# Optimization experiments

Hardware: AMD Instinct MI355X
Metric: run time of the kernel (lower is better)

Reference implementation:

```python
import jax, jax.numpy as jnp
import numpy as np

B, L, E, H = 2, 4096, 1024, 16
D = E // H          # head_dim = 64
CHUNK = 256         # matches the torch module's chunk_size


def setup_inputs() -> dict:
    key = jax.random.key(0)
    k1, k2, k3 = jax.random.split(key, 3)
    x = jax.random.normal(k1, (B, L, E), dtype=jnp.float32)
    # torch Linear weight layout: (out_features, in_features); y = x @ W.T
    W_qkv = jax.random.normal(k2, (3 * E, E), dtype=jnp.float32) * 0.02
    W_out = jax.random.normal(k3, (E, E), dtype=jnp.float32) * 0.02
    return {"x": x, "W_qkv": W_qkv, "W_out": W_out}


def _linear_attention(x, W_qkv, W_out):
    Bz, Lz, Ez = x.shape
    scale = D ** (-0.5)
    qkv = x @ W_qkv.T                                # [B, L, 3E]
    qkv = qkv.reshape(Bz, Lz, 3, H, D).transpose(2, 0, 3, 1, 4)  # [3, B, H, L, D]
    q, k, v = qkv[0], qkv[1], qkv[2]
    # feature map: elu(x) + 1, query also scaled by head_dim^-0.5
    q = (jax.nn.elu(q) + 1.0) * scale
    k = jax.nn.elu(k) + 1.0

    nc = Lz // CHUNK  # seq_len chosen divisible by CHUNK
    def to_chunks(t):  # [B,H,L,D] -> [nc, B, H, CHUNK, D]
        return t.reshape(Bz, H, nc, CHUNK, D).transpose(2, 0, 1, 3, 4)
    qc, kc, vc = to_chunks(q), to_chunks(k), to_chunks(v)

    causal = jnp.tril(jnp.ones((CHUNK, CHUNK), dtype=x.dtype))

    def step(carry, inp):
        S, Z = carry                     # S: [B,H,D,D], Z: [B,H,D]
        qi, ki, vi = inp                 # each [B,H,CHUNK,D]
        # intra-chunk causal contribution (same math as cumsum of k v^T outer products)
        attn = jnp.einsum('bhld,bhmd->bhlm', qi, ki) * causal
        num = jnp.einsum('bhlm,bhme->bhle', attn, vi) + jnp.einsum('bhld,bhde->bhle', qi, S)
        den = attn.sum(-1) + jnp.einsum('bhld,bhd->bhl', qi, Z)
        S = S + jnp.einsum('bhmd,bhme->bhde', ki, vi)
        Z = Z + ki.sum(axis=2)
        return (S, Z), (num, den)

    S0 = jnp.zeros((Bz, H, D, D), dtype=x.dtype)
    Z0 = jnp.zeros((Bz, H, D), dtype=x.dtype)
    _, (num, den) = jax.lax.scan(step, (S0, Z0), (qc, kc, vc))
    # [nc,B,H,CHUNK,D] -> [B,H,L,D]
    num = num.transpose(1, 2, 0, 3, 4).reshape(Bz, H, Lz, D)
    den = den.transpose(1, 2, 0, 3).reshape(Bz, H, Lz)
    den = jnp.maximum(den, 1e-6)
    out = num / den[..., None]
    out = out.transpose(0, 2, 1, 3).reshape(Bz, Lz, Ez)
    return out @ W_out.T


def reference(x, W_qkv, W_out):
    return _linear_attention(x, W_qkv, W_out)
```

## Files before the change

### kernel.cpp

```cpp
#include <hip/hip_runtime.h>
#include <hip/hip_bf16.h>
#include <math.h>

#define B_ 2
#define L_ 4096
#define E_ 1024
#define H_ 16
#define D_ 64
#define CK_ 64
#define NC_ 64

typedef __bf16 bf16x8 __attribute__((ext_vector_type(8)));
typedef __bf16 bf16x4 __attribute__((ext_vector_type(4)));
typedef float  f32x4  __attribute__((ext_vector_type(4)));

__device__ __forceinline__ float fmap1(float x) { return x > 0.f ? x + 1.f : expf(x); }
__device__ __forceinline__ float b2f(__bf16 v) {
    __hip_bfloat16 h = *reinterpret_cast<__hip_bfloat16*>(&v); return __bfloat162float(h);
}
__device__ __forceinline__ __bf16 f2b(float f) {
    __hip_bfloat16 h = __float2bfloat16(f); return *reinterpret_cast<__bf16*>(&h);
}
__device__ __forceinline__ unsigned short f2u(float f) {
    __hip_bfloat16 h = __float2bfloat16(f); return *reinterpret_cast<unsigned short*>(&h);
}

union U8 { bf16x8 v; __bf16 e[8]; bf16x4 half2[2]; };

__device__ __forceinline__ void async16(const __bf16* g, __bf16* lds) {
    __builtin_amdgcn_global_load_lds(
        (const __attribute__((address_space(1))) void*)g,
        (__attribute__((address_space(3))) void*)lds, 16, 0, 0);
}

__global__ __launch_bounds__(256) void cast_f32_bf16(const float* __restrict__ in,
                                                     __hip_bfloat16* __restrict__ out, int n) {
    int i = (blockIdx.x * 256 + threadIdx.x) << 2;
    if (i < n) {
        float4 v = *(const float4*)(in + i);
        ushort4 o = {f2u(v.x), f2u(v.y), f2u(v.z), f2u(v.w)};
        *(ushort4*)(out + i) = o;
    }
}

#define WVMC(n) do { asm volatile("s_waitcnt vmcnt(" #n ")" ::: "memory"); \
    __builtin_amdgcn_sched_barrier(0); } while (0)

template<int EPI>
__global__ __launch_bounds__(256) void gemm_mfma3(const __bf16* __restrict__ A,
                                                  const __bf16* __restrict__ Bw,
                                                  void* __restrict__ Cv,
                                                  __hip_bfloat16* __restrict__ KT,
                                                  __hip_bfloat16* __restrict__ VT,
                                                  int M, int N, int K) {
    __shared__ alignas(16) __bf16 As[3][128 * 32];
    __shared__ alignas(16) __bf16 Bs[3][128 * 32];
    const int tid = threadIdx.x;
    const int wave = tid >> 6, lane = tid & 63;
    const int wm = wave >> 1, wn = wave & 1;
    const int lq = lane >> 4, lr = lane & 15;
    const int m0 = blockIdx.y * 128, n0 = blockIdx.x * 128;
    const int NS = K >> 5;

    f32x4 acc[4][4];
#pragma unroll
    for (int i = 0; i < 4; ++i)
#pragma unroll
        for (int j = 0; j < 4; ++j) acc[i][j] = (f32x4){0.f, 0.f, 0.f, 0.f};

    const int stg_r = lane >> 2, stg_c = (lane & 3) << 3;
    const __bf16* Ag0 = A + (size_t)(m0 + (wave << 4) + stg_r) * K + stg_c;
    const __bf16* Ag1 = A + (size_t)(m0 + 64 + (wave << 4) + stg_r) * K + stg_c;
    const __bf16* Bg0 = Bw + (size_t)(n0 + (wave << 4) + stg_r) * K + stg_c;
    const __bf16* Bg1 = Bw + (size_t)(n0 + 64 + (wave << 4) + stg_r) * K + stg_c;
    const int dl0 = (wave << 9), dl1 = ((wave + 4) << 9);

#define STG3(bi, t) do { const int ko_ = (t) << 5; \
    async16(Ag0 + ko_, &As[bi][dl0]); \
    async16(Ag1 + ko_, &As[bi][dl1]); \
    async16(Bg0 + ko_, &Bs[bi][dl0]); \
    async16(Bg1 + ko_, &Bs[bi][dl1]); } while (0)

    STG3(0, 0);
    STG3(1, 1);
    WVMC(4);
    __builtin_amdgcn_s_barrier();

    int bi = 0, bn = 2;
    for (int t = 0; t < NS; ++t) {
        if (t + 2 < NS) STG3(bn, t + 2);
        bf16x8 af[4], bfr[4];
#pragma unroll
        for (int tt = 0; tt < 4; ++tt) {
            af[tt]  = *(const bf16x8*)&As[bi][((wm << 6) + (tt << 4) + lr) * 32 + (lq << 3)];
            bfr[tt] = *(const bf16x8*)&Bs[bi][((wn << 6) + (tt << 4) + lr) * 32 + (lq << 3)];
        }
#pragma unroll
        for (int mt = 0; mt < 4; ++mt)
#pragma unroll
            for (int nt = 0; nt < 4; ++nt)
                acc[mt][nt] = __builtin_amdgcn_mfma_f32_16x16x32_bf16(
                    af[mt], bfr[nt], acc[mt][nt], 0, 0, 0);
        if (t < NS - 2)       { WVMC(4); }
        else if (t == NS - 2) { WVMC(0); }
        __builtin_amdgcn_s_barrier();
        bi = (bi == 2) ? 0 : bi + 1;
        bn = (bn == 2) ? 0 : bn + 1;
    }

#pragma unroll
    for (int mt = 0; mt < 4; ++mt) {
#pragma unroll
        for (int nt = 0; nt < 4; ++nt) {
            int m = m0 + (wm << 6) + (mt << 4) + (lq << 2);
            int n = n0 + (wn << 6) + (nt << 4) + lr;
            if (EPI == 1) {
                int w = n >> 10, hh = (n >> 6) & 15, dd = n & 63;
                float vv[4];
#pragma unroll
                for (int r = 0; r < 4; ++r) {
                    float v = acc[mt][nt][r];
                    if (w == 0)      v = fmap1(v) * 0.125f;
                    else if (w == 1) v = fmap1(v);
                    vv[r] = v;
                    ((__hip_bfloat16*)Cv)[(size_t)(m + r) * N + n] = __float2bfloat16(v);
                }
                if (w >= 1) {
                    int b = m >> 12, l = m & 4095;
                    __hip_bfloat16* T = (w == 1) ? KT : VT;
                    ushort4 u = {f2u(vv[0]), f2u(vv[1]), f2u(vv[2]), f2u(vv[3])};
                    *(ushort4*)&T[((size_t)((b * 16 + hh) * 64 + dd) << 12) + l] = u;
                }
            } else {
#pragma unroll
                for (int r = 0; r < 4; ++r)
                    ((float*)Cv)[(size_t)(m + r) * N + n] = acc[mt][nt][r];
            }
        }
    }
#undef STG3
}

__global__ __launch_bounds__(256) void chunk_state_mfma(const __hip_bfloat16* __restrict__ KTh,
                                                        const __hip_bfloat16* __restrict__ VTh,
                                                        __hip_bfloat16* __restrict__ Sb,
                                                        __hip_bfloat16* __restrict__ Zb) {
    const int tid = threadIdx.x, wave = tid >> 6, lane = tid & 63;
    const int quad = lane >> 4, lr = lane & 15;
    const int bh = blockIdx.y;
    const int c = blockIdx.x * 4 + wave;
    const __bf16* KT = (const __bf16*)KTh;
    const __bf16* VT = (const __bf16*)VTh;

    bf16x8 vt[4][2], kt[4][2];
#pragma unroll
    for (int t = 0; t < 4; ++t)
#pragma unroll
        for (int kk = 0; kk < 2; ++kk) {
            size_t rowoff = ((size_t)(bh * 64 + t * 16 + lr) << 12) + c * CK_ + kk * 32 + quad * 8;
            vt[t][kk] = *(const bf16x8*)&VT[rowoff];
            kt[t][kk] = *(const bf16x8*)&KT[rowoff];
        }

    U8 of;
#pragma unroll
    for (int j = 0; j < 8; ++j) of.e[j] = f2b(1.0f);

    __hip_bfloat16* Sp = Sb + ((size_t)(c * 32 + bh) << 12);
#pragma unroll
    for (int es = 0; es < 4; ++es) {
#pragma unroll
        for (int dt = 0; dt < 4; ++dt) {
            f32x4 acc = (f32x4){0.f, 0.f, 0.f, 0.f};
            acc = __builtin_amdgcn_mfma_f32_16x16x32_bf16(vt[es][0], kt[dt][0], acc, 0, 0, 0);
            acc = __builtin_amdgcn_mfma_f32_16x16x32_bf16(vt[es][1], kt[dt][1], acc, 0, 0, 0);
#pragma unroll
            for (int r = 0; r < 4; ++r)
                Sp[(es * 16 + quad * 4 + r) * 64 + dt * 16 + lr] =
                    __float2bfloat16(acc[r]);
        }
    }
#pragma unroll
    for (int dt = 0; dt < 4; ++dt) {
        f32x4 z = (f32x4){0.f, 0.f, 0.f, 0.f};
        z = __builtin_amdgcn_mfma_f32_16x16x32_bf16(kt[dt][0], of.v, z, 0, 0, 0);
        z = __builtin_amdgcn_mfma_f32_16x16x32_bf16(kt[dt][1], of.v, z, 0, 0, 0);
        if (lr == 0) {
#pragma unroll
            for (int r = 0; r < 4; ++r)
                Zb[((c * 32 + bh) << 6) + dt * 16 + quad * 4 + r] = __float2bfloat16(z[r]);
        }
    }
}

__global__ __launch_bounds__(256) void prefix64(__hip_bfloat16* __restrict__ Sb,
                                                __hip_bfloat16* __restrict__ Zb) {
    const int bh = blockIdx.y;
    const int idx = blockIdx.x * 256 + threadIdx.x;
    float run = 0.f;
    for (int c = 0; c < NC_; ++c) {
        size_t off = ((size_t)(c * 32 + bh) << 12) + idx;
        float cur = __bfloat162float(Sb[off]);
        Sb[off] = __float2bfloat16(run);
        run += cur;
    }
    if (blockIdx.x == 0 && threadIdx.x < 64) {
        float zr = 0.f;
        for (int c = 0; c < NC_; ++c) {
            int zoff = ((c * 32 + bh) << 6) + threadIdx.x;
            float cz = __bfloat162float(Zb[zoff]);
            Zb[zoff] = __float2bfloat16(zr);
            zr += cz;
        }
    }
}

__global__ __launch_bounds__(256) void attn_out_mfma(const __hip_bfloat16* __restrict__ qvh,
                                                     const __hip_bfloat16* __restrict__ Sbh,
                                                     const __hip_bfloat16* __restrict__ Zbh,
                                                     const __hip_bfloat16* __restrict__ VTh,
                                                     __hip_bfloat16* __restrict__ attn) {
    __shared__ __bf16 Pbuf[4 * 64 * 68];
    const int tid = threadIdx.x, wave = tid >> 6, lane = tid & 63;
    const int quad = lane >> 4, lr = lane & 15;
    const int bh = blockIdx.y, b = bh >> 4, h = bh & 15;
    const int c = blockIdx.x * 4 + wave;
    const size_t t0 = (size_t)b * L_ + c * CK_;
    const __bf16* qb = (const __bf16*)qvh;
    const __bf16* Sb = (const __bf16*)Sbh;
    const __bf16* Zb = (const __bf16*)Zbh;
    const __bf16* VT = (const __bf16*)VTh;
    __bf16* P = Pbuf + wave * (64 * 68);

    bf16x8 qf[4][2];
#pragma unroll
    for (int ls = 0; ls < 4; ++ls)
#pragma unroll
        for (int kk = 0; kk < 2; ++kk)
            qf[ls][kk] = *(const bf16x8*)&qb[(t0 + ls * 16 + lr) * 3072 + h * 64 + kk * 32 + quad * 8];

    f32x4 num[4][4], den[4];
#pragma unroll
    for (int i = 0; i < 4; ++i) {
        den[i] = (f32x4){0.f, 0.f, 0.f, 0.f};
#pragma unroll
        for (int j = 0; j < 4; ++j) num[i][j] = (f32x4){0.f, 0.f, 0.f, 0.f};
    }

    bf16x8 zf[2];
#pragma unroll
    for (int kk = 0; kk < 2; ++kk)
        zf[kk] = *(const bf16x8*)&Zb[((size_t)(c * 32 + bh) << 6) + kk * 32 + quad * 8];
#pragma unroll
    for (int ls = 0; ls < 4; ++ls)
#pragma unroll
        for (int kk = 0; kk < 2; ++kk)
            den[ls] = __builtin_amdgcn_mfma_f32_16x16x32_bf16(qf[ls][kk], zf[kk], den[ls], 0, 0, 0);

#pragma unroll
    for (int es = 0; es < 4; ++es) {
        bf16x8 sf[2];
#pragma unroll
        for (int kk = 0; kk < 2; ++kk)
            sf[kk] = *(const bf16x8*)&Sb[((size_t)(c * 32 + bh) << 12)
                                         + (es * 16 + lr) * 64 + kk * 32 + quad * 8];
#pragma unroll
        for (int ls = 0; ls < 4; ++ls)
#pragma unroll
            for (int kk = 0; kk < 2; ++kk)
                num[ls][es] = __builtin_amdgcn_mfma_f32_16x16x32_bf16(
                    qf[ls][kk], sf[kk], num[ls][es], 0, 0, 0);
    }

    bf16x8 kf[4][2];
#pragma unroll
    for (int ms = 0; ms < 4; ++ms)
#pragma unroll
        for (int kk = 0; kk < 2; ++kk)
            kf[ms][kk] = *(const bf16x8*)&qb[(t0 + ms * 16 + lr) * 3072 + 1024 + h * 64 + kk * 32 + quad * 8];

#pragma unroll
    for (int ls = 0; ls < 4; ++ls) {
#pragma unroll
        for (int ms = 0; ms < 4; ++ms) {
            int off = (ls * 16 + lr) * 68 + ms * 16 + quad * 4;
            if (ms <= ls) {
                f32x4 pt = (f32x4){0.f, 0.f, 0.f, 0.f};
                pt = __builtin_amdgcn_mfma_f32_16x16x32_bf16(kf[ms][0], qf[ls][0], pt, 0, 0, 0);
                pt = __builtin_amdgcn_mfma_f32_16x16x32_bf16(kf[ms][1], qf[ls][1], pt, 0, 0, 0);
                ushort4 u;
                if (ms == ls) {
                    u.x = (quad * 4 + 0 > lr) ? 0 : f2u(pt[0]);
                    u.y = (quad * 4 + 1 > lr) ? 0 : f2u(pt[1]);
                    u.z = (quad * 4 + 2 > lr) ? 0 : f2u(pt[2]);
                    u.w = (quad * 4 + 3 > lr) ? 0 : f2u(pt[3]);
                } else {
                    u = (ushort4){f2u(pt[0]), f2u(pt[1]), f2u(pt[2]), f2u(pt[3])};
                }
                *(ushort4*)&P[off] = u;
            } else {
                *(ushort4*)&P[off] = (ushort4){0, 0, 0, 0};
            }
        }
    }

    U8 of;
#pragma unroll
    for (int j = 0; j < 8; ++j) of.e[j] = f2b(1.0f);

#pragma unroll
    for (int kk = 0; kk < 2; ++kk) {
        U8 pf[4];
#pragma unroll
        for (int ls = 0; ls < 4; ++ls) {
            pf[ls].half2[0] = *(const bf16x4*)&P[(ls * 16 + lr) * 68 + kk * 32 + quad * 8];
            pf[ls].half2[1] = *(const bf16x4*)&P[(ls * 16 + lr) * 68 + kk * 32 + quad * 8 + 4];
        }
        bf16x8 vf[4];
#pragma unroll
        for (int es = 0; es < 4; ++es)
            vf[es] = *(const bf16x8*)&VT[((size_t)((b * 16 + h) * 64 + es * 16 + lr) << 12)
                                         + c * CK_ + kk * 32 + quad * 8];
#pragma unroll
        for (int ls = 0; ls < 4; ++ls) {
            den[ls] = __builtin_amdgcn_mfma_f32_16x16x32_bf16(pf[ls].v, of.v, den[ls], 0, 0, 0);
#pragma unroll
            for (int es = 0; es < 4; ++es)
                num[ls][es] = __builtin_amdgcn_mfma_f32_16x16x32_bf16(
                    pf[ls].v, vf[es], num[ls][es], 0, 0, 0);
        }
    }

#pragma unroll
    for (int ls = 0; ls < 4; ++ls) {
#pragma unroll
        for (int r = 0; r < 4; ++r) {
            float inv = 1.f / fmaxf(den[ls][r], 1e-6f);
            size_t row = (t0 + ls * 16 + quad * 4 + r) * 1024 + h * 64;
#pragma unroll
            for (int es = 0; es < 4; ++es)
                attn[row + es * 16 + lr] = __float2bfloat16(num[ls][es][r] * inv);
        }
    }
}

extern "C" void kernel_launch(void* const* d_in, const int* in_sizes, int n_in,
                              void* d_out, int out_size, void* d_ws, size_t ws_size,
                              hipStream_t stream) {
    (void)ws_size; (void)out_size;
    const float *x = nullptr, *Wqkv = nullptr, *Wout = nullptr;
    for (int i = 0; i < n_in; ++i) {
        if (in_sizes[i] == 8388608)      x    = (const float*)d_in[i];
        else if (in_sizes[i] == 3145728) Wqkv = (const float*)d_in[i];
        else if (in_sizes[i] == 1048576) Wout = (const float*)d_in[i];
    }

    __hip_bfloat16* ws16  = (__hip_bfloat16*)d_ws;
    __hip_bfloat16* xb    = ws16;
    __hip_bfloat16* attn  = ws16;
    __hip_bfloat16* Wqkvb = ws16 + 8388608;
    __hip_bfloat16* Woutb = Wqkvb + 3145728;
    __hip_bfloat16* qv    = Woutb + 1048576;
    __hip_bfloat16* VT    = qv + 25165824;
    __hip_bfloat16* KT    = VT + 8388608;
    __hip_bfloat16* Sb    = KT + 8388608;
    __hip_bfloat16* Zb    = Sb + 8388608;

    cast_f32_bf16<<<8388608 / 1024, 256, 0, stream>>>(x, xb, 8388608);
    cast_f32_bf16<<<3145728 / 1024, 256, 0, stream>>>(Wqkv, Wqkvb, 3145728);
    cast_f32_bf16<<<1048576 / 1024, 256, 0, stream>>>(Wout, Woutb, 1048576);

    gemm_mfma3<1><<<dim3(3072 / 128, 8192 / 128), 256, 0, stream>>>(
        (const __bf16*)xb, (const __bf16*)Wqkvb, qv, KT, VT, B_ * L_, 3 * E_, E_);
    chunk_state_mfma<<<dim3(16, B_ * H_), 256, 0, stream>>>(KT, VT, Sb, Zb);
    prefix64<<<dim3(16, B_ * H_), 256, 0, stream>>>(Sb, Zb);
    attn_out_mfma<<<dim3(16, B_ * H_), 256, 0, stream>>>(qv, Sb, Zb, VT, attn);
    gemm_mfma3<0><<<dim3(1024 / 128, 8192 / 128), 256, 0, stream>>>(
        (const __bf16*)attn, (const __bf16*)Woutb, d_out, nullptr, nullptr, B_ * L_, E_, E_);
}
```

Before: 244.4 us.

## Load GEMM B operand directly to registers, drop V row-major store, batch prefix loads

The GEMM no longer stages the weight (B) tile through LDS. Each wave loads its B fragments straight from global memory into registers, double-buffered across K steps, while A keeps the async LDS triple buffer. The QKV epilogue now skips writing V into the row-major qkv buffer, since only VT is consumed downstream. The prefix-scan kernel loads all 64 chunk values into registers before writing, so loads are no longer serialized, and launch bounds now ask for 4 blocks per CU. In exchange, B reads become uncached, strided global loads with no LDS sharing between the waves that need the same columns, and register pressure rises.

```diff
diff --git a/kernel.cpp b/kernel.cpp
--- a/kernel.cpp
+++ b/kernel.cpp
@@ -15,9 +15,6 @@
 typedef float  f32x4  __attribute__((ext_vector_type(4)));
 
 __device__ __forceinline__ float fmap1(float x) { return x > 0.f ? x + 1.f : expf(x); }
-__device__ __forceinline__ float b2f(__bf16 v) {
-    __hip_bfloat16 h = *reinterpret_cast<__hip_bfloat16*>(&v); return __bfloat162float(h);
-}
 __device__ __forceinline__ __bf16 f2b(float f) {
     __hip_bfloat16 h = __float2bfloat16(f); return *reinterpret_cast<__bf16*>(&h);
 }
@@ -47,14 +44,13 @@
     __builtin_amdgcn_sched_barrier(0); } while (0)
 
 template<int EPI>
-__global__ __launch_bounds__(256) void gemm_mfma3(const __bf16* __restrict__ A,
+__global__ __launch_bounds__(256, 4) void gemm_bd(const __bf16* __restrict__ A,
                                                   const __bf16* __restrict__ Bw,
                                                   void* __restrict__ Cv,
                                                   __hip_bfloat16* __restrict__ KT,
                                                   __hip_bfloat16* __restrict__ VT,
                                                   int M, int N, int K) {
     __shared__ alignas(16) __bf16 As[3][128 * 32];
-    __shared__ alignas(16) __bf16 Bs[3][128 * 32];
     const int tid = threadIdx.x;
     const int wave = tid >> 6, lane = tid & 63;
     const int wm = wave >> 1, wn = wave & 1;
@@ -71,41 +67,49 @@
     const int stg_r = lane >> 2, stg_c = (lane & 3) << 3;
     const __bf16* Ag0 = A + (size_t)(m0 + (wave << 4) + stg_r) * K + stg_c;
     const __bf16* Ag1 = A + (size_t)(m0 + 64 + (wave << 4) + stg_r) * K + stg_c;
-    const __bf16* Bg0 = Bw + (size_t)(n0 + (wave << 4) + stg_r) * K + stg_c;
-    const __bf16* Bg1 = Bw + (size_t)(n0 + 64 + (wave << 4) + stg_r) * K + stg_c;
     const int dl0 = (wave << 9), dl1 = ((wave + 4) << 9);
 
-#define STG3(bi, t) do { const int ko_ = (t) << 5; \
+    const __bf16* Bp = Bw + (size_t)(n0 + (wn << 6) + lr) * K + (lq << 3);
+
+#define STGA(bi, t) do { const int ko_ = (t) << 5; \
     async16(Ag0 + ko_, &As[bi][dl0]); \
-    async16(Ag1 + ko_, &As[bi][dl1]); \
-    async16(Bg0 + ko_, &Bs[bi][dl0]); \
-    async16(Bg1 + ko_, &Bs[bi][dl1]); } while (0)
-
-    STG3(0, 0);
-    STG3(1, 1);
-    WVMC(4);
+    async16(Ag1 + ko_, &As[bi][dl1]); } while (0)
+#define LDB(dst, t) { const int ko_ = (t) << 5; \
+    _Pragma("unroll") for (int tt = 0; tt < 4; ++tt) \
+        dst[tt] = *(const bf16x8*)&Bp[(size_t)(tt << 4) * K + ko_]; }
+#define LDA_MM(breg) { \
+    bf16x8 af[4]; \
+    _Pragma("unroll") for (int tt = 0; tt < 4; ++tt) \
+        af[tt] = *(const bf16x8*)&As[bi][((wm << 6) + (tt << 4) + lr) * 32 + (lq << 3)]; \
+    _Pragma("unroll") for (int mt = 0; mt < 4; ++mt) \
+    _Pragma("unroll") for (int nt = 0; nt < 4; ++nt) \
+        acc[mt][nt] = __builtin_amdgcn_mfma_f32_16x16x32_bf16( \
+            af[mt], breg[nt], acc[mt][nt], 0, 0, 0); }
+#define ENDSTEP(t) do { \
+    if ((t) < NS - 2)       { WVMC(6); } \
+    else if ((t) == NS - 2) { WVMC(4); } \
+    __builtin_amdgcn_s_barrier(); \
+    bi = (bi == 2) ? 0 : bi + 1; \
+    bn = (bn == 2) ? 0 : bn + 1; } while (0)
+
+    bf16x8 bA[4], bB[4];
+
+    LDB(bA, 0);
+    STGA(0, 0);
+    STGA(1, 1);
+    WVMC(2);
     __builtin_amdgcn_s_barrier();
 
     int bi = 0, bn = 2;
-    for (int t = 0; t < NS; ++t) {
-        if (t + 2 < NS) STG3(bn, t + 2);
-        bf16x8 af[4], bfr[4];
-#pragma unroll
-        for (int tt = 0; tt < 4; ++tt) {
-            af[tt]  = *(const bf16x8*)&As[bi][((wm << 6) + (tt << 4) + lr) * 32 + (lq << 3)];
-            bfr[tt] = *(const bf16x8*)&Bs[bi][((wn << 6) + (tt << 4) + lr) * 32 + (lq << 3)];
-        }
-#pragma unroll
-        for (int mt = 0; mt < 4; ++mt)
-#pragma unroll
-            for (int nt = 0; nt < 4; ++nt)
-                acc[mt][nt] = __builtin_amdgcn_mfma_f32_16x16x32_bf16(
-                    af[mt], bfr[nt], acc[mt][nt], 0, 0, 0);
-        if (t < NS - 2)       { WVMC(4); }
-        else if (t == NS - 2) { WVMC(0); }
-        __builtin_amdgcn_s_barrier();
-        bi = (bi == 2) ? 0 : bi + 1;
-        bn = (bn == 2) ? 0 : bn + 1;
+    for (int t = 0; t < NS; t += 2) {
+        if (t + 1 < NS) LDB(bB, t + 1);
+        if (t + 2 < NS) STGA(bn, t + 2);
+        LDA_MM(bA);
+        ENDSTEP(t);
+        if (t + 2 < NS) LDB(bA, t + 2);
+        if (t + 3 < NS) STGA(bn, t + 3);
+        LDA_MM(bB);
+        ENDSTEP(t + 1);
     }
 
 #pragma unroll
@@ -123,7 +127,8 @@
                     if (w == 0)      v = fmap1(v) * 0.125f;
                     else if (w == 1) v = fmap1(v);
                     vv[r] = v;
-                    ((__hip_bfloat16*)Cv)[(size_t)(m + r) * N + n] = __float2bfloat16(v);
+                    if (w <= 1)
+                        ((__hip_bfloat16*)Cv)[(size_t)(m + r) * N + n] = __float2bfloat16(v);
                 }
                 if (w >= 1) {
                     int b = m >> 12, l = m & 4095;
@@ -138,7 +143,10 @@
             }
         }
     }
-#undef STG3
+#undef STGA
+#undef LDB
+#undef LDA_MM
+#undef ENDSTEP
 }
 
 __global__ __launch_bounds__(256) void chunk_state_mfma(const __hip_bfloat16* __restrict__ KTh,
@@ -197,20 +205,26 @@
                                                 __hip_bfloat16* __restrict__ Zb) {
     const int bh = blockIdx.y;
     const int idx = blockIdx.x * 256 + threadIdx.x;
+    float v[NC_];
+#pragma unroll
+    for (int c = 0; c < NC_; ++c)
+        v[c] = __bfloat162float(Sb[((size_t)(c * 32 + bh) << 12) + idx]);
     float run = 0.f;
+#pragma unroll
     for (int c = 0; c < NC_; ++c) {
-        size_t off = ((size_t)(c * 32 + bh) << 12) + idx;
-        float cur = __bfloat162float(Sb[off]);
-        Sb[off] = __float2bfloat16(run);
-        run += cur;
+        Sb[((size_t)(c * 32 + bh) << 12) + idx] = __float2bfloat16(run);
+        run += v[c];
     }
     if (blockIdx.x == 0 && threadIdx.x < 64) {
+        float z[NC_];
+#pragma unroll
+        for (int c = 0; c < NC_; ++c)
+            z[c] = __bfloat162float(Zb[((c * 32 + bh) << 6) + threadIdx.x]);
         float zr = 0.f;
+#pragma unroll
         for (int c = 0; c < NC_; ++c) {
-            int zoff = ((c * 32 + bh) << 6) + threadIdx.x;
-            float cz = __bfloat162float(Zb[zoff]);
-            Zb[zoff] = __float2bfloat16(zr);
-            zr += cz;
+            Zb[((c * 32 + bh) << 6) + threadIdx.x] = __float2bfloat16(zr);
+            zr += z[c];
         }
     }
 }
@@ -370,11 +384,11 @@
     cast_f32_bf16<<<3145728 / 1024, 256, 0, stream>>>(Wqkv, Wqkvb, 3145728);
     cast_f32_bf16<<<1048576 / 1024, 256, 0, stream>>>(Wout, Woutb, 1048576);
 
-    gemm_mfma3<1><<<dim3(3072 / 128, 8192 / 128), 256, 0, stream>>>(
+    gemm_bd<1><<<dim3(3072 / 128, 8192 / 128), 256, 0, stream>>>(
         (const __bf16*)xb, (const __bf16*)Wqkvb, qv, KT, VT, B_ * L_, 3 * E_, E_);
     chunk_state_mfma<<<dim3(16, B_ * H_), 256, 0, stream>>>(KT, VT, Sb, Zb);
     prefix64<<<dim3(16, B_ * H_), 256, 0, stream>>>(Sb, Zb);
     attn_out_mfma<<<dim3(16, B_ * H_), 256, 0, stream>>>(qv, Sb, Zb, VT, attn);
-    gemm_mfma3<0><<<dim3(1024 / 128, 8192 / 128), 256, 0, stream>>>(
+    gemm_bd<0><<<dim3(1024 / 128, 8192 / 128), 256, 0, stream>>>(
         (const __bf16*)attn, (const __bf16*)Woutb, d_out, nullptr, nullptr, B_ * L_, E_, E_);
 }
```

Measured after the change: 289.1 us. +18.3%, slower.

## Swizzle GEMM block order, skip unused V row-major store, batch prefix loads

Applied to the files above, without the earlier changes.

Remaps GEMM workgroup IDs so consecutive blocks are grouped per XCD (an 8-way interleave), which is meant to improve L2 reuse of A/B tiles. The QKV epilogue no longer writes V into the row-major output, since V is only consumed via the transposed VT buffer. The prefix-sum kernel now issues all 64 chunk loads up front into registers before the serial scan, exposing memory-level parallelism instead of a dependent load/store chain. The remap assumes the block count is divisible by 8, and the register arrays raise VGPR pressure.

```diff
diff --git a/kernel.cpp b/kernel.cpp
--- a/kernel.cpp
+++ b/kernel.cpp
@@ -15,9 +15,6 @@
 typedef float  f32x4  __attribute__((ext_vector_type(4)));
 
 __device__ __forceinline__ float fmap1(float x) { return x > 0.f ? x + 1.f : expf(x); }
-__device__ __forceinline__ float b2f(__bf16 v) {
-    __hip_bfloat16 h = *reinterpret_cast<__hip_bfloat16*>(&v); return __bfloat162float(h);
-}
 __device__ __forceinline__ __bf16 f2b(float f) {
     __hip_bfloat16 h = __float2bfloat16(f); return *reinterpret_cast<__bf16*>(&h);
 }
@@ -59,7 +56,14 @@
     const int wave = tid >> 6, lane = tid & 63;
     const int wm = wave >> 1, wn = wave & 1;
     const int lq = lane >> 4, lr = lane & 15;
-    const int m0 = blockIdx.y * 128, n0 = blockIdx.x * 128;
+
+    const int nwg = gridDim.x * gridDim.y;
+    const int bid = blockIdx.y * gridDim.x + blockIdx.x;
+    const int cpx = nwg >> 3;
+    const int wgid = (bid & 7) * cpx + (bid >> 3);
+    const int bx = wgid % gridDim.x, by = wgid / gridDim.x;
+    const int m0 = by * 128, n0 = bx * 128;
+
     const int NS = K >> 5;
 
     f32x4 acc[4][4];
@@ -123,7 +127,8 @@
                     if (w == 0)      v = fmap1(v) * 0.125f;
                     else if (w == 1) v = fmap1(v);
                     vv[r] = v;
-                    ((__hip_bfloat16*)Cv)[(size_t)(m + r) * N + n] = __float2bfloat16(v);
+                    if (w <= 1)
+                        ((__hip_bfloat16*)Cv)[(size_t)(m + r) * N + n] = __float2bfloat16(v);
                 }
                 if (w >= 1) {
                     int b = m >> 12, l = m & 4095;
@@ -197,20 +202,26 @@
                                                 __hip_bfloat16* __restrict__ Zb) {
     const int bh = blockIdx.y;
     const int idx = blockIdx.x * 256 + threadIdx.x;
+    float v[NC_];
+#pragma unroll
+    for (int c = 0; c < NC_; ++c)
+        v[c] = __bfloat162float(Sb[((size_t)(c * 32 + bh) << 12) + idx]);
     float run = 0.f;
+#pragma unroll
     for (int c = 0; c < NC_; ++c) {
-        size_t off = ((size_t)(c * 32 + bh) << 12) + idx;
-        float cur = __bfloat162float(Sb[off]);
-        Sb[off] = __float2bfloat16(run);
-        run += cur;
+        Sb[((size_t)(c * 32 + bh) << 12) + idx] = __float2bfloat16(run);
+        run += v[c];
     }
     if (blockIdx.x == 0 && threadIdx.x < 64) {
+        float z[NC_];
+#pragma unroll
+        for (int c = 0; c < NC_; ++c)
+            z[c] = __bfloat162float(Zb[((c * 32 + bh) << 6) + threadIdx.x]);
         float zr = 0.f;
+#pragma unroll
         for (int c = 0; c < NC_; ++c) {
-            int zoff = ((c * 32 + bh) << 6) + threadIdx.x;
-            float cz = __bfloat162float(Zb[zoff]);
-            Zb[zoff] = __float2bfloat16(zr);
-            zr += cz;
+            Zb[((c * 32 + bh) << 6) + threadIdx.x] = __float2bfloat16(zr);
+            zr += z[c];
         }
     }
 }
```

Result: faster. 232.8 us (-4.7%).
